# Kernel tuning notes

Measured on AMD Instinct MI355X. Metric: run time of the kernel, lower is better.

## Reference

```python
import jax, jax.numpy as jnp
import numpy as np

BETA = 0.25      # commitment loss weight
DECAY = 0.99     # EMA decay
EPS = 1e-5       # Laplace smoothing for counts


def setup_inputs() -> dict:
    key = jax.random.key(0)
    k1, k2, k3 = jax.random.split(key, 3)
    B, d, h, w, K = 16, 64, 64, 64, 1024
    z_e = jax.random.normal(k1, (B, d, h, w), dtype=jnp.float32)
    codebook = jax.random.normal(k2, (K, d), dtype=jnp.float32)
    ema_count = jnp.ones((K,), dtype=jnp.float32)
    ema_sum = jax.random.normal(k3, (K, d), dtype=jnp.float32)
    return {"z_e": z_e, "codebook": codebook, "ema_count": ema_count, "ema_sum": ema_sum}


def reference(z_e, codebook, ema_count, ema_sum):
    B, d, h, w = z_e.shape
    K = codebook.shape[0]
    # [B,d,h,w] -> [N,d], N = B*h*w
    z_flat = jnp.transpose(z_e, (0, 2, 3, 1)).reshape(-1, d)
    # squared euclidean distances [N,K]
    dist = (jnp.sum(z_flat * z_flat, axis=1, keepdims=True)
            - 2.0 * (z_flat @ codebook.T)
            + jnp.sum(codebook * codebook, axis=1)[None, :])
    indices = jnp.argmin(dist, axis=1)                      # [N] int
    e_k = codebook[indices].reshape(B, h, w, d).transpose(0, 3, 1, 2)  # [B,d,h,w]

    # --- EMA codebook update (training mode, no grad) ---
    zf = jax.lax.stop_gradient(z_flat)
    counts = jax.ops.segment_sum(jnp.ones((zf.shape[0],), dtype=zf.dtype), indices, num_segments=K)
    sums = jax.ops.segment_sum(zf, indices, num_segments=K)
    new_count = ema_count * DECAY + (1.0 - DECAY) * counts
    new_sum = ema_sum * DECAY + (1.0 - DECAY) * sums
    n = jnp.sum(new_count)
    count_s = (new_count + EPS) / (n + K * EPS) * n
    new_codebook = new_sum / count_s[:, None]

    # straight-through estimator
    e_k_ste = z_e + jax.lax.stop_gradient(e_k - z_e)
    L_commit = (jnp.mean((z_e - jax.lax.stop_gradient(e_k)) ** 2)
                + BETA * jnp.mean((jax.lax.stop_gradient(z_e) - e_k) ** 2))
    return (e_k_ste, indices.reshape(B, h, w), L_commit, new_codebook, new_count, new_sum)
```

## Files before the change

kernel.cpp:

```cpp
#include <hip/hip_runtime.h>
#include <hip/hip_bf16.h>
#include <hip/hip_fp16.h>

#define NB 16
#define DD 64
#define HW 4096
#define NTOT 65536
#define KC 1024

#define O_EK   0
#define O_IDX  4194304
#define O_L    4259840
#define O_CB   4259841
#define O_CNT  4325377
#define O_SUM  4326401

#define WS_IDX    0
#define WS_LCPART 65536
#define WS_N      66048
#define WS_CNORM  66560
#define WS_PSUM   67584
#define WS_PCNT   329728
#define WS_CBH    399360
#define WS_CBL    432128

#define MARGIN 0.002f

typedef _Float16 v8h __attribute__((ext_vector_type(8)));
typedef float    v4f __attribute__((ext_vector_type(4)));

__global__ __launch_bounds__(256) void k_pre(const float* __restrict__ cb,
                                             const float* __restrict__ ema_count,
                                             float* __restrict__ cnorm,
                                             float* __restrict__ n_ws,
                                             unsigned short* __restrict__ cbh,
                                             unsigned short* __restrict__ cbl) {
    const int t = threadIdx.x;
    const int w = (blockIdx.x * 256 + t) >> 6;
    const int l = t & 63;
    float s = 0.f;
    if (l < 16) {
        float4 v = *(const float4*)(cb + (size_t)w * DD + l * 4);
        s = v.x * v.x + v.y * v.y + v.z * v.z + v.w * v.w;
    }
#pragma unroll
    for (int m = 1; m <= 8; m <<= 1) s += __shfl_xor(s, m, 64);
    if (l == 0) cnorm[w] = s;

    const int e4 = blockIdx.x * 256 + t;
    if (e4 < 16384) {
        float4 v4 = ((const float4*)cb)[e4];
        __half hx = __float2half(v4.x), hy = __float2half(v4.y),
               hz = __float2half(v4.z), hw2 = __float2half(v4.w);
        ushort4 h4 = { __half_as_ushort(hx), __half_as_ushort(hy),
                       __half_as_ushort(hz), __half_as_ushort(hw2) };
        ((ushort4*)cbh)[e4] = h4;
        ushort4 l4 = { __half_as_ushort(__float2half(v4.x - __half2float(hx))),
                       __half_as_ushort(__float2half(v4.y - __half2float(hy))),
                       __half_as_ushort(__float2half(v4.z - __half2float(hz))),
                       __half_as_ushort(__float2half(v4.w - __half2float(hw2))) };
        ((ushort4*)cbl)[e4] = l4;
    }

    if (blockIdx.x == 0) {
        __shared__ float red[256];
        red[t] = ema_count[t] + ema_count[t + 256] + ema_count[t + 512] + ema_count[t + 768];
        __syncthreads();
        for (int s2 = 128; s2 >= 1; s2 >>= 1) {
            if (t < s2) red[t] += red[t + s2];
            __syncthreads();
        }
        if (t == 0) n_ws[0] = 0.99f * red[0] + 0.01f * 65536.0f;
    }
}

__global__ __launch_bounds__(256) void k_argmin(const float* __restrict__ z_e,
                                                const float* __restrict__ cbf,
                                                const unsigned short* __restrict__ cbh,
                                                const unsigned short* __restrict__ cbl,
                                                const float* __restrict__ cnorm,
                                                int* __restrict__ idx_ws,
                                                float* __restrict__ out) {
    __shared__ __align__(16) unsigned short A2h[8][128][8];
    __shared__ __align__(16) unsigned short A2l[8][128][8];
    __shared__ __align__(16) unsigned short B2h[2][8][64][8];
    __shared__ __align__(16) unsigned short B2l[2][8][64][8];
    __shared__ int idx_lds[128];
    __shared__ int flagrows[128];
    __shared__ int flagi1[128];
    __shared__ int flagi2[128];
    __shared__ int nflag;

    float* slab = (float*)&B2h[0][0][0][0];

    const int t  = threadIdx.x;
    const int n0 = blockIdx.x * 128;
    const int b   = n0 >> 12;
    const int hw0 = n0 & 4095;
    const float* zbase = z_e + (size_t)b * (DD * HW) + hw0;

    if (t == 0) nflag = 0;

    for (int sl = 0; sl < 2; ++sl) {
        if (sl) __syncthreads();
#pragma unroll
        for (int s = 0; s < 4; ++s) {
            int idx = t + s * 256;
            int j   = idx >> 5;
            int m4  = (idx & 31) << 2;
            float4 v = *(const float4*)(zbase + (size_t)(sl * 32 + j) * HW + m4);
            *(float4*)&slab[j * 128 + m4] = v;
        }
        __syncthreads();
#pragma unroll
        for (int s = 0; s < 2; ++s) {
            int ss  = t + s * 256;
            int chl = ss >> 7;
            int m   = ss & 127;
            int ch  = sl * 4 + chl;
            unsigned hv[4], lv[4];
#pragma unroll
            for (int p = 0; p < 4; ++p) {
                float v0 = slab[(chl * 8 + 2 * p    ) * 128 + m];
                float v1 = slab[(chl * 8 + 2 * p + 1) * 128 + m];
                __half h0 = __float2half(v0), h1 = __float2half(v1);
                __half l0 = __float2half(v0 - __half2float(h0));
                __half l1 = __float2half(v1 - __half2float(h1));
                hv[p] = (unsigned)__half_as_ushort(h0) | ((unsigned)__half_as_ushort(h1) << 16);
                lv[p] = (unsigned)__half_as_ushort(l0) | ((unsigned)__half_as_ushort(l1) << 16);
            }
            uint4 hq = {hv[0], hv[1], hv[2], hv[3]};
            uint4 lq = {lv[0], lv[1], lv[2], lv[3]};
            *(uint4*)&A2h[ch][m][0] = hq;
            *(uint4*)&A2l[ch][m][0] = lq;
        }
    }
    __syncthreads();

    const int w    = t >> 6;
    const int lane = t & 63;
    const int c    = lane & 15;
    const int q    = lane >> 4;

    const int ch0   = t >> 6;
    const int code0 = t & 63;
    const int ch1   = 4 + (t >> 6);
    const int code1 = t & 63;

    v8h Afh[2][2], Afl[2][2];
#pragma unroll
    for (int g = 0; g < 2; ++g) {
        int m = 32 * w + 16 * g + c;
#pragma unroll
        for (int s = 0; s < 2; ++s) {
            Afh[g][s] = *(const v8h*)&A2h[s * 4 + q][m][0];
            Afl[g][s] = *(const v8h*)&A2l[s * 4 + q][m][0];
        }
    }

    {
        size_t g0 = ((size_t)code0) * 64 + ch0 * 8;
        size_t g1 = ((size_t)code1) * 64 + ch1 * 8;
        *(uint4*)&B2h[0][ch0][code0][0] = *(const uint4*)(cbh + g0);
        *(uint4*)&B2l[0][ch0][code0][0] = *(const uint4*)(cbl + g0);
        *(uint4*)&B2h[0][ch1][code1][0] = *(const uint4*)(cbh + g1);
        *(uint4*)&B2l[0][ch1][code1][0] = *(const uint4*)(cbl + g1);
    }
    __syncthreads();

    float m1v[2][4], m2v[2][4]; int m1i[2][4], m2i[2][4];
#pragma unroll
    for (int g = 0; g < 2; ++g)
#pragma unroll
        for (int r = 0; r < 4; ++r) {
            m1v[g][r] = 3.4e38f; m2v[g][r] = 3.4e38f;
            m1i[g][r] = 0;       m2i[g][r] = 0;
        }

    for (int kt = 0; kt < 16; ++kt) {
        const int cur = kt & 1, nxt = cur ^ 1;
        uint4 ph0, pl0, ph1, pl1;
        if (kt < 15) {
            size_t g0 = ((size_t)((kt + 1) * 64 + code0)) * 64 + ch0 * 8;
            size_t g1 = ((size_t)((kt + 1) * 64 + code1)) * 64 + ch1 * 8;
            ph0 = *(const uint4*)(cbh + g0);
            pl0 = *(const uint4*)(cbl + g0);
            ph1 = *(const uint4*)(cbh + g1);
            pl1 = *(const uint4*)(cbl + g1);
        }

#pragma unroll
        for (int sub = 0; sub < 4; ++sub) {
            const int cl = sub * 16 + c;
            v8h Bfh0 = *(const v8h*)&B2h[cur][q][cl][0];
            v8h Bfh1 = *(const v8h*)&B2h[cur][4 + q][cl][0];
            v8h Bfl0 = *(const v8h*)&B2l[cur][q][cl][0];
            v8h Bfl1 = *(const v8h*)&B2l[cur][4 + q][cl][0];
            const int kg = kt * 64 + cl;
            float cnc = cnorm[kg];
#pragma unroll
            for (int g = 0; g < 2; ++g) {
                v4f acc = {0.f, 0.f, 0.f, 0.f};
                acc = __builtin_amdgcn_mfma_f32_16x16x32_f16(Afh[g][0], Bfh0, acc, 0, 0, 0);
                acc = __builtin_amdgcn_mfma_f32_16x16x32_f16(Afh[g][1], Bfh1, acc, 0, 0, 0);
                acc = __builtin_amdgcn_mfma_f32_16x16x32_f16(Afh[g][0], Bfl0, acc, 0, 0, 0);
                acc = __builtin_amdgcn_mfma_f32_16x16x32_f16(Afh[g][1], Bfl1, acc, 0, 0, 0);
                acc = __builtin_amdgcn_mfma_f32_16x16x32_f16(Afl[g][0], Bfh0, acc, 0, 0, 0);
                acc = __builtin_amdgcn_mfma_f32_16x16x32_f16(Afl[g][1], Bfh1, acc, 0, 0, 0);
#pragma unroll
                for (int r = 0; r < 4; ++r) {
                    float v = fmaf(-2.0f, acc[r], cnc);
                    bool b1 = v < m1v[g][r];
                    bool bs = v < m2v[g][r];
                    float nm2v = b1 ? m1v[g][r] : (bs ? v  : m2v[g][r]);
                    int   nm2i = b1 ? m1i[g][r] : (bs ? kg : m2i[g][r]);
                    m1i[g][r] = b1 ? kg : m1i[g][r];
                    m1v[g][r] = b1 ? v  : m1v[g][r];
                    m2v[g][r] = nm2v;
                    m2i[g][r] = nm2i;
                }
            }
        }

        if (kt < 15) {
            *(uint4*)&B2h[nxt][ch0][code0][0] = ph0;
            *(uint4*)&B2l[nxt][ch0][code0][0] = pl0;
            *(uint4*)&B2h[nxt][ch1][code1][0] = ph1;
            *(uint4*)&B2l[nxt][ch1][code1][0] = pl1;
        }
        __syncthreads();
    }

#pragma unroll
    for (int g = 0; g < 2; ++g)
#pragma unroll
        for (int r = 0; r < 4; ++r) {
            float a = m1v[g][r];  int ii = m1i[g][r];
            float b2 = m2v[g][r]; int i2 = m2i[g][r];
#pragma unroll
            for (int mask = 1; mask <= 8; mask <<= 1) {
                float o1  = __shfl_xor(a,  mask, 64);
                int   oi  = __shfl_xor(ii, mask, 64);
                float o2  = __shfl_xor(b2, mask, 64);
                int   o2i = __shfl_xor(i2, mask, 64);
                bool take = (o1 < a) || (o1 == a && oi < ii);
                float loserV = take ? a  : o1;
                int   loserI = take ? ii : oi;
                bool c2 = (o2 < b2);
                float cv = c2 ? o2  : b2;
                int   ci = c2 ? o2i : i2;
                bool l2 = (loserV < cv);
                b2 = l2 ? loserV : cv;
                i2 = l2 ? loserI : ci;
                a  = take ? o1 : a;
                ii = take ? oi : ii;
            }
            if (c == 0) {
                int row = 32 * w + 16 * g + q * 4 + r;
                idx_lds[row] = ii;
                if ((b2 - a) < MARGIN) {
                    int p = atomicAdd(&nflag, 1);
                    flagrows[p] = row; flagi1[p] = ii; flagi2[p] = i2;
                }
            }
        }
    __syncthreads();

    {
        int nf = nflag;
        for (int f = w; f < nf; f += 4) {
            int row = flagrows[f], i1 = flagi1[f], i2x = flagi2[f];
            const float* zrow = z_e + (size_t)b * (DD * HW) + hw0 + row;
            float zj = zrow[(size_t)lane * HW];
            float p1 = zj * cbf[(size_t)i1  * DD + lane];
            float p2 = zj * cbf[(size_t)i2x * DD + lane];
#pragma unroll
            for (int mask = 1; mask <= 32; mask <<= 1) {
                p1 += __shfl_xor(p1, mask, 64);
                p2 += __shfl_xor(p2, mask, 64);
            }
            if (lane == 0) {
                float d1 = fmaf(-2.0f, p1, cnorm[i1]);
                float d2 = fmaf(-2.0f, p2, cnorm[i2x]);
                if (d2 < d1 || (d2 == d1 && i2x < i1)) idx_lds[row] = i2x;
            }
        }
    }
    __syncthreads();

    if (t < 128) {
        int bi = idx_lds[t];
        out[O_IDX + n0 + t] = (float)bi;
        idx_ws[n0 + t] = bi;
    }
}

__global__ __launch_bounds__(1024) void k_out(const int* __restrict__ idx_ws,
                                              const float* __restrict__ z_e,
                                              const float* __restrict__ cb,
                                              float* __restrict__ psum,
                                              int* __restrict__ pcnt,
                                              float* __restrict__ lc_part,
                                              float* __restrict__ out) {
    __shared__ float acc[KC];
    __shared__ int bins[KC];
    __shared__ float cbj[KC];
    __shared__ float lcr[16];
    const int j = blockIdx.x & 63;
    const int c = blockIdx.x >> 6;
    const int t = threadIdx.x;
    acc[t] = 0.f;
    bins[t] = 0;
    cbj[t] = cb[(size_t)t * DD + j];
    __syncthreads();
    const float* zj = z_e + (size_t)j * HW;
    float* oj = out + O_EK + (size_t)j * HW;
    const int base = c * 16384;
    float lc = 0.f;
#pragma unroll
    for (int i = 0; i < 4; ++i) {
        int n4 = base + i * 4096 + t * 4;
        int b = n4 >> 12, hw = n4 & 4095;
        size_t zoff = (size_t)b * (DD * HW) + hw;
        float4 z4 = *(const float4*)(zj + zoff);
        int4   k4 = *(const int4*)(idx_ws + n4);
        float e0 = cbj[k4.x], e1 = cbj[k4.y], e2 = cbj[k4.z], e3 = cbj[k4.w];
        float4 o4 = { z4.x + (e0 - z4.x), z4.y + (e1 - z4.y),
                      z4.z + (e2 - z4.z), z4.w + (e3 - z4.w) };
        *(float4*)(oj + zoff) = o4;
        float d0 = z4.x - e0, d1 = z4.y - e1, d2 = z4.z - e2, d3 = z4.w - e3;
        lc = fmaf(d0, d0, lc); lc = fmaf(d1, d1, lc);
        lc = fmaf(d2, d2, lc); lc = fmaf(d3, d3, lc);
        atomicAdd(&acc[k4.x], z4.x);
        atomicAdd(&acc[k4.y], z4.y);
        atomicAdd(&acc[k4.z], z4.z);
        atomicAdd(&acc[k4.w], z4.w);
        if (j == 0) {
            atomicAdd(&bins[k4.x], 1); atomicAdd(&bins[k4.y], 1);
            atomicAdd(&bins[k4.z], 1); atomicAdd(&bins[k4.w], 1);
        }
    }
    __syncthreads();
    psum[(size_t)c * 65536 + j * 1024 + t] = acc[t];
    if (j == 0) pcnt[c * 1024 + t] = bins[t];
#pragma unroll
    for (int m = 32; m >= 1; m >>= 1) lc += __shfl_xor(lc, m, 64);
    if ((t & 63) == 0) lcr[t >> 6] = lc;
    __syncthreads();
    if (t == 0) {
        float s = 0.f;
#pragma unroll
        for (int u = 0; u < 16; ++u) s += lcr[u];
        lc_part[blockIdx.x] = s;
    }
}

__global__ __launch_bounds__(1024) void k_epi(const float* __restrict__ psum,
                                              const int* __restrict__ pcnt,
                                              const float* __restrict__ ema_sum,
                                              const float* __restrict__ ema_count,
                                              const float* __restrict__ n_ws,
                                              const float* __restrict__ lc_part,
                                              float* __restrict__ out) {
    const int t = threadIdx.x;
    const int e = blockIdx.x * 1024 + t;
    const int k = e >> 6, j = e & 63;
    float s4 = psum[j * 1024 + k] + psum[65536 + j * 1024 + k]
             + psum[131072 + j * 1024 + k] + psum[196608 + j * 1024 + k];
    float ns = ema_sum[e] * 0.99f + 0.01f * s4;
    out[O_SUM + e] = ns;
    int cnt = pcnt[k] + pcnt[1024 + k] + pcnt[2048 + k] + pcnt[3072 + k];
    float nc = ema_count[k] * 0.99f + 0.01f * (float)cnt;
    float n  = n_ws[0];
    float cs = (nc + 1e-5f) / (n + 1024.0f * 1e-5f) * n;
    out[O_CB + e] = ns / cs;
    if (blockIdx.x == 0) {
        int c2 = pcnt[t] + pcnt[1024 + t] + pcnt[2048 + t] + pcnt[3072 + t];
        out[O_CNT + t] = ema_count[t] * 0.99f + 0.01f * (float)c2;
    }
    if (blockIdx.x == 1) {
        __shared__ float red[512];
        if (t < 512) red[t] = (t < 256) ? lc_part[t] : 0.f;
        __syncthreads();
        for (int s = 256; s >= 1; s >>= 1) {
            if (t < s) red[t] += red[t + s];
            __syncthreads();
        }
        if (t == 0) out[O_L] = 1.25f * red[0] * (1.0f / 4194304.0f);
    }
}

extern "C" void kernel_launch(void* const* d_in, const int* in_sizes, int n_in,
                              void* d_out, int out_size, void* d_ws, size_t ws_size,
                              hipStream_t stream) {
    const float* z_e       = (const float*)d_in[0];
    const float* cb        = (const float*)d_in[1];
    const float* ema_count = (const float*)d_in[2];
    const float* ema_sum   = (const float*)d_in[3];
    float* out             = (float*)d_out;

    float* ws_f      = (float*)d_ws;
    int*   idx_ws    = (int*)d_ws;
    float* lc_part   = ws_f + WS_LCPART;
    float* n_ws      = ws_f + WS_N;
    float* cnorm_ws  = ws_f + WS_CNORM;
    float* psum      = ws_f + WS_PSUM;
    int*   pcnt      = (int*)(ws_f + WS_PCNT);
    unsigned short* cbh = (unsigned short*)(ws_f + WS_CBH);
    unsigned short* cbl = (unsigned short*)(ws_f + WS_CBL);

    k_pre<<<256, 256, 0, stream>>>(cb, ema_count, cnorm_ws, n_ws, cbh, cbl);
    k_argmin<<<NTOT / 128, 256, 0, stream>>>(z_e, cb, cbh, cbl, cnorm_ws, idx_ws, out);
    k_out<<<256, 1024, 0, stream>>>(idx_ws, z_e, cb, psum, pcnt, lc_part, out);
    k_epi<<<64, 1024, 0, stream>>>(psum, pcnt, ema_sum, ema_count, n_ws, lc_part, out);
}
```

Baseline: 146.4 us.

## Pack argmin index into distance bits and double threads per argmin block

Result: faster. 139.1 us (-5.0%).

```diff
diff --git a/kernel.cpp b/kernel.cpp
--- a/kernel.cpp
+++ b/kernel.cpp
@@ -24,10 +24,9 @@
 #define WS_CBH    399360
 #define WS_CBL    432128
 
-#define MARGIN 0.002f
-
 typedef _Float16 v8h __attribute__((ext_vector_type(8)));
 typedef float    v4f __attribute__((ext_vector_type(4)));
+typedef unsigned short ush;
 
 __global__ __launch_bounds__(256) void k_pre(const float* __restrict__ cb,
                                              const float* __restrict__ ema_count,
@@ -74,65 +73,60 @@
     }
 }
 
-__global__ __launch_bounds__(256) void k_argmin(const float* __restrict__ z_e,
+__global__ __launch_bounds__(512) void k_argmin(const float* __restrict__ z_e,
                                                 const float* __restrict__ cbf,
                                                 const unsigned short* __restrict__ cbh,
                                                 const unsigned short* __restrict__ cbl,
                                                 const float* __restrict__ cnorm,
                                                 int* __restrict__ idx_ws,
                                                 float* __restrict__ out) {
-    __shared__ __align__(16) unsigned short A2h[8][128][8];
-    __shared__ __align__(16) unsigned short A2l[8][128][8];
-    __shared__ __align__(16) unsigned short B2h[2][8][64][8];
-    __shared__ __align__(16) unsigned short B2l[2][8][64][8];
+    __shared__ __align__(16) unsigned char ldsAB[32768];
+    __shared__ __align__(16) float slab[2048];
     __shared__ int idx_lds[128];
     __shared__ int flagrows[128];
     __shared__ int flagi1[128];
     __shared__ int flagi2[128];
     __shared__ int nflag;
 
-    float* slab = (float*)&B2h[0][0][0][0];
+    ush (*A2h)[128][8]  = (ush(*)[128][8])(ldsAB);
+    ush (*A2l)[128][8]  = (ush(*)[128][8])(ldsAB + 16384);
+    ush (*B2h)[8][64][8] = (ush(*)[8][64][8])(ldsAB);
+    ush (*B2l)[8][64][8] = (ush(*)[8][64][8])(ldsAB + 16384);
 
     const int t  = threadIdx.x;
     const int n0 = blockIdx.x * 128;
-    const int b   = n0 >> 12;
+    const int bb  = n0 >> 12;
     const int hw0 = n0 & 4095;
-    const float* zbase = z_e + (size_t)b * (DD * HW) + hw0;
+    const float* zbase = z_e + (size_t)bb * (DD * HW) + hw0;
 
     if (t == 0) nflag = 0;
 
-    for (int sl = 0; sl < 2; ++sl) {
-        if (sl) __syncthreads();
-#pragma unroll
-        for (int s = 0; s < 4; ++s) {
-            int idx = t + s * 256;
-            int j   = idx >> 5;
-            int m4  = (idx & 31) << 2;
-            float4 v = *(const float4*)(zbase + (size_t)(sl * 32 + j) * HW + m4);
-            *(float4*)&slab[j * 128 + m4] = v;
-        }
-        __syncthreads();
-#pragma unroll
-        for (int s = 0; s < 2; ++s) {
-            int ss  = t + s * 256;
-            int chl = ss >> 7;
-            int m   = ss & 127;
-            int ch  = sl * 4 + chl;
-            unsigned hv[4], lv[4];
-#pragma unroll
-            for (int p = 0; p < 4; ++p) {
-                float v0 = slab[(chl * 8 + 2 * p    ) * 128 + m];
-                float v1 = slab[(chl * 8 + 2 * p + 1) * 128 + m];
+    {
+        const int jr   = t >> 5;
+        const int m4   = (t & 31) << 2;
+        const int chl  = t >> 8;
+        const int cm   = t & 127;
+        const int half = (t >> 7) & 1;
+        for (int sl = 0; sl < 4; ++sl) {
+            if (sl) __syncthreads();
+            float4 v = *(const float4*)(zbase + (size_t)(sl * 16 + jr) * HW + m4);
+            *(float4*)&slab[jr * 128 + m4] = v;
+            __syncthreads();
+            unsigned hv[2], lv[2];
+#pragma unroll
+            for (int p = 0; p < 2; ++p) {
+                int jj = chl * 8 + half * 4 + p * 2;
+                float v0 = slab[jj * 128 + cm];
+                float v1 = slab[(jj + 1) * 128 + cm];
                 __half h0 = __float2half(v0), h1 = __float2half(v1);
                 __half l0 = __float2half(v0 - __half2float(h0));
                 __half l1 = __float2half(v1 - __half2float(h1));
                 hv[p] = (unsigned)__half_as_ushort(h0) | ((unsigned)__half_as_ushort(h1) << 16);
                 lv[p] = (unsigned)__half_as_ushort(l0) | ((unsigned)__half_as_ushort(l1) << 16);
             }
-            uint4 hq = {hv[0], hv[1], hv[2], hv[3]};
-            uint4 lq = {lv[0], lv[1], lv[2], lv[3]};
-            *(uint4*)&A2h[ch][m][0] = hq;
-            *(uint4*)&A2l[ch][m][0] = lq;
+            uint2 hq = {hv[0], hv[1]}, lq = {lv[0], lv[1]};
+            *(uint2*)&A2h[sl * 2 + chl][cm][half * 4] = hq;
+            *(uint2*)&A2l[sl * 2 + chl][cm][half * 4] = lq;
         }
     }
     __syncthreads();
@@ -142,51 +136,38 @@
     const int c    = lane & 15;
     const int q    = lane >> 4;
 
+    v8h Afh[2], Afl[2];
+    {
+        int m = 16 * w + c;
+#pragma unroll
+        for (int s = 0; s < 2; ++s) {
+            Afh[s] = *(const v8h*)&A2h[s * 4 + q][m][0];
+            Afl[s] = *(const v8h*)&A2l[s * 4 + q][m][0];
+        }
+    }
+    __syncthreads();
+
     const int ch0   = t >> 6;
     const int code0 = t & 63;
-    const int ch1   = 4 + (t >> 6);
-    const int code1 = t & 63;
-
-    v8h Afh[2][2], Afl[2][2];
-#pragma unroll
-    for (int g = 0; g < 2; ++g) {
-        int m = 32 * w + 16 * g + c;
-#pragma unroll
-        for (int s = 0; s < 2; ++s) {
-            Afh[g][s] = *(const v8h*)&A2h[s * 4 + q][m][0];
-            Afl[g][s] = *(const v8h*)&A2l[s * 4 + q][m][0];
-        }
-    }
 
     {
         size_t g0 = ((size_t)code0) * 64 + ch0 * 8;
-        size_t g1 = ((size_t)code1) * 64 + ch1 * 8;
         *(uint4*)&B2h[0][ch0][code0][0] = *(const uint4*)(cbh + g0);
         *(uint4*)&B2l[0][ch0][code0][0] = *(const uint4*)(cbl + g0);
-        *(uint4*)&B2h[0][ch1][code1][0] = *(const uint4*)(cbh + g1);
-        *(uint4*)&B2l[0][ch1][code1][0] = *(const uint4*)(cbl + g1);
-    }
-    __syncthreads();
-
-    float m1v[2][4], m2v[2][4]; int m1i[2][4], m2i[2][4];
-#pragma unroll
-    for (int g = 0; g < 2; ++g)
-#pragma unroll
-        for (int r = 0; r < 4; ++r) {
-            m1v[g][r] = 3.4e38f; m2v[g][r] = 3.4e38f;
-            m1i[g][r] = 0;       m2i[g][r] = 0;
-        }
+    }
+    __syncthreads();
+
+    float m1f[4], m2f[4];
+#pragma unroll
+    for (int r = 0; r < 4; ++r) { m1f[r] = 3.4e38f; m2f[r] = 3.4e38f; }
 
     for (int kt = 0; kt < 16; ++kt) {
         const int cur = kt & 1, nxt = cur ^ 1;
-        uint4 ph0, pl0, ph1, pl1;
+        uint4 ph0, pl0;
         if (kt < 15) {
             size_t g0 = ((size_t)((kt + 1) * 64 + code0)) * 64 + ch0 * 8;
-            size_t g1 = ((size_t)((kt + 1) * 64 + code1)) * 64 + ch1 * 8;
             ph0 = *(const uint4*)(cbh + g0);
             pl0 = *(const uint4*)(cbl + g0);
-            ph1 = *(const uint4*)(cbh + g1);
-            pl1 = *(const uint4*)(cbl + g1);
         }
 
 #pragma unroll
@@ -196,81 +177,63 @@
             v8h Bfh1 = *(const v8h*)&B2h[cur][4 + q][cl][0];
             v8h Bfl0 = *(const v8h*)&B2l[cur][q][cl][0];
             v8h Bfl1 = *(const v8h*)&B2l[cur][4 + q][cl][0];
-            const int kg = kt * 64 + cl;
+            const unsigned kg = (unsigned)(kt * 64 + cl);
             float cnc = cnorm[kg];
-#pragma unroll
-            for (int g = 0; g < 2; ++g) {
-                v4f acc = {0.f, 0.f, 0.f, 0.f};
-                acc = __builtin_amdgcn_mfma_f32_16x16x32_f16(Afh[g][0], Bfh0, acc, 0, 0, 0);
-                acc = __builtin_amdgcn_mfma_f32_16x16x32_f16(Afh[g][1], Bfh1, acc, 0, 0, 0);
-                acc = __builtin_amdgcn_mfma_f32_16x16x32_f16(Afh[g][0], Bfl0, acc, 0, 0, 0);
-                acc = __builtin_amdgcn_mfma_f32_16x16x32_f16(Afh[g][1], Bfl1, acc, 0, 0, 0);
-                acc = __builtin_amdgcn_mfma_f32_16x16x32_f16(Afl[g][0], Bfh0, acc, 0, 0, 0);
-                acc = __builtin_amdgcn_mfma_f32_16x16x32_f16(Afl[g][1], Bfh1, acc, 0, 0, 0);
-#pragma unroll
-                for (int r = 0; r < 4; ++r) {
-                    float v = fmaf(-2.0f, acc[r], cnc);
-                    bool b1 = v < m1v[g][r];
-                    bool bs = v < m2v[g][r];
-                    float nm2v = b1 ? m1v[g][r] : (bs ? v  : m2v[g][r]);
-                    int   nm2i = b1 ? m1i[g][r] : (bs ? kg : m2i[g][r]);
-                    m1i[g][r] = b1 ? kg : m1i[g][r];
-                    m1v[g][r] = b1 ? v  : m1v[g][r];
-                    m2v[g][r] = nm2v;
-                    m2i[g][r] = nm2i;
-                }
+            v4f acc = {0.f, 0.f, 0.f, 0.f};
+            acc = __builtin_amdgcn_mfma_f32_16x16x32_f16(Afh[0], Bfh0, acc, 0, 0, 0);
+            acc = __builtin_amdgcn_mfma_f32_16x16x32_f16(Afh[1], Bfh1, acc, 0, 0, 0);
+            acc = __builtin_amdgcn_mfma_f32_16x16x32_f16(Afh[0], Bfl0, acc, 0, 0, 0);
+            acc = __builtin_amdgcn_mfma_f32_16x16x32_f16(Afh[1], Bfl1, acc, 0, 0, 0);
+            acc = __builtin_amdgcn_mfma_f32_16x16x32_f16(Afl[0], Bfh0, acc, 0, 0, 0);
+            acc = __builtin_amdgcn_mfma_f32_16x16x32_f16(Afl[1], Bfh1, acc, 0, 0, 0);
+#pragma unroll
+            for (int r = 0; r < 4; ++r) {
+                float v = fmaf(-2.0f, acc[r], cnc);
+                unsigned vu = (__float_as_uint(v) & 0xFFFFFC00u) | kg;
+                float vp = __uint_as_float(vu);
+                m2f[r] = fminf(m2f[r], fmaxf(m1f[r], vp));
+                m1f[r] = fminf(m1f[r], vp);
             }
         }
 
         if (kt < 15) {
             *(uint4*)&B2h[nxt][ch0][code0][0] = ph0;
             *(uint4*)&B2l[nxt][ch0][code0][0] = pl0;
-            *(uint4*)&B2h[nxt][ch1][code1][0] = ph1;
-            *(uint4*)&B2l[nxt][ch1][code1][0] = pl1;
         }
         __syncthreads();
     }
 
 #pragma unroll
-    for (int g = 0; g < 2; ++g)
-#pragma unroll
-        for (int r = 0; r < 4; ++r) {
-            float a = m1v[g][r];  int ii = m1i[g][r];
-            float b2 = m2v[g][r]; int i2 = m2i[g][r];
-#pragma unroll
-            for (int mask = 1; mask <= 8; mask <<= 1) {
-                float o1  = __shfl_xor(a,  mask, 64);
-                int   oi  = __shfl_xor(ii, mask, 64);
-                float o2  = __shfl_xor(b2, mask, 64);
-                int   o2i = __shfl_xor(i2, mask, 64);
-                bool take = (o1 < a) || (o1 == a && oi < ii);
-                float loserV = take ? a  : o1;
-                int   loserI = take ? ii : oi;
-                bool c2 = (o2 < b2);
-                float cv = c2 ? o2  : b2;
-                int   ci = c2 ? o2i : i2;
-                bool l2 = (loserV < cv);
-                b2 = l2 ? loserV : cv;
-                i2 = l2 ? loserI : ci;
-                a  = take ? o1 : a;
-                ii = take ? oi : ii;
-            }
-            if (c == 0) {
-                int row = 32 * w + 16 * g + q * 4 + r;
-                idx_lds[row] = ii;
-                if ((b2 - a) < MARGIN) {
-                    int p = atomicAdd(&nflag, 1);
-                    flagrows[p] = row; flagi1[p] = ii; flagi2[p] = i2;
-                }
-            }
-        }
+    for (int r = 0; r < 4; ++r) {
+        float a = m1f[r], b2 = m2f[r];
+#pragma unroll
+        for (int mask = 1; mask <= 8; mask <<= 1) {
+            float o1 = __shfl_xor(a, mask, 64);
+            float o2 = __shfl_xor(b2, mask, 64);
+            float mx = fmaxf(a, o1);
+            a  = fminf(a, o1);
+            b2 = fminf(fminf(b2, o2), mx);
+        }
+        if (c == 0) {
+            int row = 16 * w + q * 4 + r;
+            int i1 = (int)(__float_as_uint(a) & 1023u);
+            idx_lds[row] = i1;
+            float margin = fmaf(fabsf(a), 6e-4f, 0.0015f);
+            if (b2 - a < margin) {
+                int p = atomicAdd(&nflag, 1);
+                flagrows[p] = row;
+                flagi1[p] = i1;
+                flagi2[p] = (int)(__float_as_uint(b2) & 1023u);
+            }
+        }
+    }
     __syncthreads();
 
     {
         int nf = nflag;
-        for (int f = w; f < nf; f += 4) {
+        for (int f = w; f < nf; f += 8) {
             int row = flagrows[f], i1 = flagi1[f], i2x = flagi2[f];
-            const float* zrow = z_e + (size_t)b * (DD * HW) + hw0 + row;
+            const float* zrow = zbase + row;
             float zj = zrow[(size_t)lane * HW];
             float p1 = zj * cbf[(size_t)i1  * DD + lane];
             float p2 = zj * cbf[(size_t)i2x * DD + lane];
@@ -410,7 +373,7 @@
     unsigned short* cbl = (unsigned short*)(ws_f + WS_CBL);
 
     k_pre<<<256, 256, 0, stream>>>(cb, ema_count, cnorm_ws, n_ws, cbh, cbl);
-    k_argmin<<<NTOT / 128, 256, 0, stream>>>(z_e, cb, cbh, cbl, cnorm_ws, idx_ws, out);
+    k_argmin<<<NTOT / 128, 512, 0, stream>>>(z_e, cb, cbh, cbl, cnorm_ws, idx_ws, out);
     k_out<<<256, 1024, 0, stream>>>(idx_ws, z_e, cb, psum, pcnt, lc_part, out);
     k_epi<<<64, 1024, 0, stream>>>(psum, pcnt, ema_sum, ema_count, n_ws, lc_part, out);
 }
```
